# Optimization experiments

Measured on AMD Instinct MI355X. Metric: run time of the kernel, lower is better.

Reference implementation:

```python
import jax, jax.numpy as jnp
import numpy as np

S, NB, C = 7, 2, 20
LAMBDA_COORD, LAMBDA_NOOBJ = 5.0, 0.5
EPS = 1e-6


def _iou(a, b):
    """Midpoint-format IoU. a, b: [..., 4] = (x, y, w, h)."""
    ax1, ay1 = a[..., 0] - a[..., 2] / 2, a[..., 1] - a[..., 3] / 2
    ax2, ay2 = a[..., 0] + a[..., 2] / 2, a[..., 1] + a[..., 3] / 2
    bx1, by1 = b[..., 0] - b[..., 2] / 2, b[..., 1] - b[..., 3] / 2
    bx2, by2 = b[..., 0] + b[..., 2] / 2, b[..., 1] + b[..., 3] / 2
    iw = jnp.clip(jnp.minimum(ax2, bx2) - jnp.maximum(ax1, bx1), 0.0)
    ih = jnp.clip(jnp.minimum(ay2, by2) - jnp.maximum(ay1, by1), 0.0)
    inter = iw * ih
    area_a = jnp.abs((ax2 - ax1) * (ay2 - ay1))
    area_b = jnp.abs((bx2 - bx1) * (by2 - by1))
    return inter / (area_a + area_b - inter + EPS)


def setup_inputs() -> dict:
    key = jax.random.key(0)
    k1, k2, k3, k4 = jax.random.split(key, 4)
    N = 16384
    predictions = jax.random.uniform(k1, (N, S * S * (C + NB * 5)), dtype=jnp.float32)
    cls = jax.random.uniform(k2, (N, S, S, C), dtype=jnp.float32)
    box_rest = jax.random.uniform(k3, (N, S, S, 4), dtype=jnp.float32)  # y,w,h,conf
    u = jax.random.uniform(k4, (N, S, S, 2), dtype=jnp.float32)
    flag = jnp.where(u[..., 0] < 0.3, 1.0, u[..., 1] * 0.99)
    targets = jnp.concatenate([cls, flag[..., None], box_rest], axis=-1)  # [N,S,S,25]
    return {"predictions": predictions, "targets": targets}


def reference(predictions, targets):
    N = predictions.shape[0]
    pred = predictions.reshape(N, S, S, C + NB * 5)
    class_pred = pred[..., :C]                      # [N,S,S,20]
    b1 = pred[..., C:C + 5]                         # [N,S,S,5]
    b2 = pred[..., C + 5:C + 10]                    # [N,S,S,5]
    tbox = targets[..., C:C + 5]                    # [N,S,S,5]
    obj = (targets[..., C] == 1.0).astype(pred.dtype)  # [N,S,S]

    iou1 = _iou(b1[..., :4], tbox[..., :4])
    iou2 = _iou(b2[..., :4], tbox[..., :4])
    resp = jnp.where((iou1 > iou2)[..., None], b1, b2)  # responsible box [N,S,S,5]

    xy = (resp[..., 0] - tbox[..., 0]) ** 2 + (resp[..., 1] - tbox[..., 1]) ** 2
    wh = (jnp.sqrt(resp[..., 2]) - jnp.sqrt(tbox[..., 2])) ** 2 \
       + (jnp.sqrt(resp[..., 3]) - jnp.sqrt(tbox[..., 3])) ** 2
    coord = LAMBDA_COORD * (xy + wh)
    conf = (resp[..., 4] - tbox[..., 4]) ** 2
    cls_loss = jnp.sum((class_pred - targets[..., :C]) ** 2, axis=-1)

    obj_terms = jnp.sum(obj * (coord + conf + cls_loss))
    noobj_terms = LAMBDA_NOOBJ * jnp.sum((1.0 - obj) * (b1[..., 4] ** 2 + b2[..., 4] ** 2))
    return (obj_terms + noobj_terms) / N
```

## Files before the change

kernel.cpp:

```cpp
#include <hip/hip_runtime.h>
#include <math.h>

#define SS 7
#define CC 20
#define CELL_PRED 30
#define CELL_TGT  25
#define BLOCK 256

__device__ __forceinline__ float iou_box(const float* __restrict__ a,
                                         const float* __restrict__ b) {
    const float EPS = 1e-6f;
    float ax1 = a[0] - a[2] * 0.5f, ay1 = a[1] - a[3] * 0.5f;
    float ax2 = a[0] + a[2] * 0.5f, ay2 = a[1] + a[3] * 0.5f;
    float bx1 = b[0] - b[2] * 0.5f, by1 = b[1] - b[3] * 0.5f;
    float bx2 = b[0] + b[2] * 0.5f, by2 = b[1] + b[3] * 0.5f;
    float iw = fmaxf(fminf(ax2, bx2) - fmaxf(ax1, bx1), 0.0f);
    float ih = fmaxf(fminf(ay2, by2) - fmaxf(ay1, by1), 0.0f);
    float inter = iw * ih;
    float area_a = fabsf((ax2 - ax1) * (ay2 - ay1));
    float area_b = fabsf((bx2 - bx1) * (by2 - by1));
    return inter / (area_a + area_b - inter + EPS);
}

__global__ __launch_bounds__(BLOCK) void yolo_cell_loss(
    const float* __restrict__ pred,
    const float* __restrict__ tgt,
    float* __restrict__ partials,
    int nCells)
{
    __shared__ __align__(16) float s_pred[BLOCK * CELL_PRED];
    __shared__ __align__(16) float s_tgt [BLOCK * CELL_TGT];
    __shared__ float s_red[BLOCK / 64];

    const int tid = threadIdx.x;
    const int blockCell = blockIdx.x * BLOCK;
    const bool fullBlock = (blockCell + BLOCK) <= nCells;

    if (fullBlock) {
        const float4* gp = (const float4*)(pred + (size_t)blockCell * CELL_PRED);
        float4* sp = (float4*)s_pred;
        #pragma unroll
        for (int i = tid; i < BLOCK * CELL_PRED / 4; i += BLOCK) sp[i] = gp[i];
        const float4* gt = (const float4*)(tgt + (size_t)blockCell * CELL_TGT);
        float4* st = (float4*)s_tgt;
        #pragma unroll
        for (int i = tid; i < BLOCK * CELL_TGT / 4; i += BLOCK) st[i] = gt[i];
    } else {
        int nc = nCells - blockCell;
        if (nc < 0) nc = 0;
        for (int i = tid; i < nc * CELL_PRED; i += BLOCK)
            s_pred[i] = pred[(size_t)blockCell * CELL_PRED + i];
        for (int i = tid; i < nc * CELL_TGT; i += BLOCK)
            s_tgt[i] = tgt[(size_t)blockCell * CELL_TGT + i];
    }
    __syncthreads();

    float loss = 0.0f;
    const int cell = blockCell + tid;
    if (cell < nCells) {
        const float* p = s_pred + tid * CELL_PRED;
        const float* t = s_tgt  + tid * CELL_TGT;

        const float* b1 = p + CC;
        const float* b2 = p + CC + 5;
        const float* tb = t + CC;

        float obj = (tb[0] == 1.0f) ? 1.0f : 0.0f;

        float iou1 = iou_box(b1, tb);
        float iou2 = iou_box(b2, tb);
        bool pick1 = iou1 > iou2;
        float r0 = pick1 ? b1[0] : b2[0];
        float r1 = pick1 ? b1[1] : b2[1];
        float r2 = pick1 ? b1[2] : b2[2];
        float r3 = pick1 ? b1[3] : b2[3];
        float r4 = pick1 ? b1[4] : b2[4];

        float dx = r0 - tb[0], dy = r1 - tb[1];
        float xy = dx * dx + dy * dy;
        float dw = sqrtf(r2) - sqrtf(tb[2]);
        float dh = sqrtf(r3) - sqrtf(tb[3]);
        float wh = dw * dw + dh * dh;
        float coord = 5.0f * (xy + wh);
        float dconf = r4 - tb[4];
        float conf = dconf * dconf;

        float cls = 0.0f;
        #pragma unroll
        for (int k = 0; k < CC; ++k) {
            float d = p[k] - t[k];
            cls += d * d;
        }

        float noobj = 0.5f * (1.0f - obj) * (b1[4] * b1[4] + b2[4] * b2[4]);
        loss = obj * (coord + conf + cls) + noobj;
    }

    #pragma unroll
    for (int off = 32; off > 0; off >>= 1)
        loss += __shfl_down(loss, off, 64);
    if ((tid & 63) == 0) s_red[tid >> 6] = loss;
    __syncthreads();
    if (tid == 0) {
        float s = 0.0f;
        #pragma unroll
        for (int w = 0; w < BLOCK / 64; ++w) s += s_red[w];
        partials[blockIdx.x] = s;
    }
}

__global__ __launch_bounds__(BLOCK) void yolo_final_reduce(
    const float* __restrict__ partials, int nPartials, double invN,
    float* __restrict__ out)
{
    __shared__ double s_red[BLOCK / 64];
    double sum = 0.0;
    for (int i = threadIdx.x; i < nPartials; i += BLOCK)
        sum += (double)partials[i];
    #pragma unroll
    for (int off = 32; off > 0; off >>= 1)
        sum += __shfl_down(sum, off, 64);
    if ((threadIdx.x & 63) == 0) s_red[threadIdx.x >> 6] = sum;
    __syncthreads();
    if (threadIdx.x == 0) {
        double s = 0.0;
        #pragma unroll
        for (int w = 0; w < BLOCK / 64; ++w) s += s_red[w];
        out[0] = (float)(s * invN);
    }
}

extern "C" void kernel_launch(void* const* d_in, const int* in_sizes, int n_in,
                              void* d_out, int out_size, void* d_ws, size_t ws_size,
                              hipStream_t stream) {
    const float* pred = (const float*)d_in[0];
    const float* tgt  = (const float*)d_in[1];
    float* out = (float*)d_out;
    float* partials = (float*)d_ws;

    const int N = in_sizes[0] / (SS * SS * CELL_PRED);
    const int nCells = N * SS * SS;
    const int nBlocks = (nCells + BLOCK - 1) / BLOCK;

    yolo_cell_loss<<<nBlocks, BLOCK, 0, stream>>>(pred, tgt, partials, nCells);
    yolo_final_reduce<<<1, BLOCK, 0, stream>>>(partials, nBlocks, 1.0 / (double)N, out);
}
```

Before: 205.7 us.

## Use persistent grid with register-prefetched tiles and fused atomic final reduction

Replaces the one-block-per-256-cells launch with a fixed grid of 1280 blocks of 128 threads that loop over 128-cell tiles. Each block prefetches the next tile into registers while computing the current one from LDS, so global loads overlap compute. The separate final-reduce kernel is dropped in favour of a double atomicAdd plus a last-block counter, with a memset added to zero the workspace. It assumes nCells is a multiple of 128 and drops tail handling, and it adds an extra memset launch.

```diff
diff --git a/kernel.cpp b/kernel.cpp
--- a/kernel.cpp
+++ b/kernel.cpp
@@ -5,7 +5,13 @@
 #define CC 20
 #define CELL_PRED 30
 #define CELL_TGT  25
-#define BLOCK 256
+#define TILE 128
+#define BLOCK 128
+#define P4_PER_TILE (TILE * CELL_PRED / 4)
+#define T4_PER_TILE (TILE * CELL_TGT / 4)
+#define NPJ 8
+#define NTJ 7
+#define GRID 1280
 
 __device__ __forceinline__ float iou_box(const float* __restrict__ a,
                                          const float* __restrict__ b) {
@@ -22,111 +28,130 @@
     return inter / (area_a + area_b - inter + EPS);
 }
 
-__global__ __launch_bounds__(BLOCK) void yolo_cell_loss(
+__global__ __launch_bounds__(BLOCK) void yolo_loss_fused(
     const float* __restrict__ pred,
     const float* __restrict__ tgt,
-    float* __restrict__ partials,
-    int nCells)
+    float* __restrict__ out,
+    double* __restrict__ accum,
+    int* __restrict__ counter,
+    int nCells, int nTiles, double invN)
 {
-    __shared__ __align__(16) float s_pred[BLOCK * CELL_PRED];
-    __shared__ __align__(16) float s_tgt [BLOCK * CELL_TGT];
-    __shared__ float s_red[BLOCK / 64];
+    __shared__ __align__(16) float s_pred[TILE * CELL_PRED];
+    __shared__ __align__(16) float s_tgt [TILE * CELL_TGT];
+    __shared__ float s_red[2];
 
     const int tid = threadIdx.x;
-    const int blockCell = blockIdx.x * BLOCK;
-    const bool fullBlock = (blockCell + BLOCK) <= nCells;
 
-    if (fullBlock) {
-        const float4* gp = (const float4*)(pred + (size_t)blockCell * CELL_PRED);
-        float4* sp = (float4*)s_pred;
+    float4 rp[NPJ], rt[NTJ];
+
+    int t = blockIdx.x;
+    {
+        const float4* gp = (const float4*)pred + (size_t)t * P4_PER_TILE;
+        const float4* gt = (const float4*)tgt + (size_t)t * T4_PER_TILE;
         #pragma unroll
-        for (int i = tid; i < BLOCK * CELL_PRED / 4; i += BLOCK) sp[i] = gp[i];
-        const float4* gt = (const float4*)(tgt + (size_t)blockCell * CELL_TGT);
-        float4* st = (float4*)s_tgt;
+        for (int j = 0; j < NPJ; ++j) {
+            int idx = tid + j * BLOCK;
+            if (idx < P4_PER_TILE) rp[j] = gp[idx];
+        }
         #pragma unroll
-        for (int i = tid; i < BLOCK * CELL_TGT / 4; i += BLOCK) st[i] = gt[i];
-    } else {
-        int nc = nCells - blockCell;
-        if (nc < 0) nc = 0;
-        for (int i = tid; i < nc * CELL_PRED; i += BLOCK)
-            s_pred[i] = pred[(size_t)blockCell * CELL_PRED + i];
-        for (int i = tid; i < nc * CELL_TGT; i += BLOCK)
-            s_tgt[i] = tgt[(size_t)blockCell * CELL_TGT + i];
+        for (int j = 0; j < NTJ; ++j) {
+            int idx = tid + j * BLOCK;
+            if (idx < T4_PER_TILE) rt[j] = gt[idx];
+        }
     }
-    __syncthreads();
 
     float loss = 0.0f;
-    const int cell = blockCell + tid;
-    if (cell < nCells) {
-        const float* p = s_pred + tid * CELL_PRED;
-        const float* t = s_tgt  + tid * CELL_TGT;
 
-        const float* b1 = p + CC;
-        const float* b2 = p + CC + 5;
-        const float* tb = t + CC;
+    while (t < nTiles) {
+        __syncthreads();
+        {
+            float4* sp = (float4*)s_pred;
+            float4* st = (float4*)s_tgt;
+            #pragma unroll
+            for (int j = 0; j < NPJ; ++j) {
+                int idx = tid + j * BLOCK;
+                if (idx < P4_PER_TILE) sp[idx] = rp[j];
+            }
+            #pragma unroll
+            for (int j = 0; j < NTJ; ++j) {
+                int idx = tid + j * BLOCK;
+                if (idx < T4_PER_TILE) st[idx] = rt[j];
+            }
+        }
+        __syncthreads();
 
-        float obj = (tb[0] == 1.0f) ? 1.0f : 0.0f;
-
-        float iou1 = iou_box(b1, tb);
-        float iou2 = iou_box(b2, tb);
-        bool pick1 = iou1 > iou2;
-        float r0 = pick1 ? b1[0] : b2[0];
-        float r1 = pick1 ? b1[1] : b2[1];
-        float r2 = pick1 ? b1[2] : b2[2];
-        float r3 = pick1 ? b1[3] : b2[3];
-        float r4 = pick1 ? b1[4] : b2[4];
-
-        float dx = r0 - tb[0], dy = r1 - tb[1];
-        float xy = dx * dx + dy * dy;
-        float dw = sqrtf(r2) - sqrtf(tb[2]);
-        float dh = sqrtf(r3) - sqrtf(tb[3]);
-        float wh = dw * dw + dh * dh;
-        float coord = 5.0f * (xy + wh);
-        float dconf = r4 - tb[4];
-        float conf = dconf * dconf;
-
-        float cls = 0.0f;
-        #pragma unroll
-        for (int k = 0; k < CC; ++k) {
-            float d = p[k] - t[k];
-            cls += d * d;
+        int tn = t + GRID;
+        if (tn < nTiles) {
+            const float4* gp = (const float4*)pred + (size_t)tn * P4_PER_TILE;
+            const float4* gt = (const float4*)tgt + (size_t)tn * T4_PER_TILE;
+            #pragma unroll
+            for (int j = 0; j < NPJ; ++j) {
+                int idx = tid + j * BLOCK;
+                if (idx < P4_PER_TILE) rp[j] = gp[idx];
+            }
+            #pragma unroll
+            for (int j = 0; j < NTJ; ++j) {
+                int idx = tid + j * BLOCK;
+                if (idx < T4_PER_TILE) rt[j] = gt[idx];
+            }
         }
 
-        float noobj = 0.5f * (1.0f - obj) * (b1[4] * b1[4] + b2[4] * b2[4]);
-        loss = obj * (coord + conf + cls) + noobj;
+        {
+            const float* p = s_pred + tid * CELL_PRED;
+            const float* tt = s_tgt + tid * CELL_TGT;
+            const float* b1 = p + CC;
+            const float* b2 = p + CC + 5;
+            const float* tb = tt + CC;
+
+            float obj = (tb[0] == 1.0f) ? 1.0f : 0.0f;
+
+            float iou1 = iou_box(b1, tb);
+            float iou2 = iou_box(b2, tb);
+            bool pick1 = iou1 > iou2;
+            float r0 = pick1 ? b1[0] : b2[0];
+            float r1 = pick1 ? b1[1] : b2[1];
+            float r2 = pick1 ? b1[2] : b2[2];
+            float r3 = pick1 ? b1[3] : b2[3];
+            float r4 = pick1 ? b1[4] : b2[4];
+
+            float dx = r0 - tb[0], dy = r1 - tb[1];
+            float xy = dx * dx + dy * dy;
+            float dw = sqrtf(r2) - sqrtf(tb[2]);
+            float dh = sqrtf(r3) - sqrtf(tb[3]);
+            float wh = dw * dw + dh * dh;
+            float coord = 5.0f * (xy + wh);
+            float dconf = r4 - tb[4];
+            float conf = dconf * dconf;
+
+            float cls = 0.0f;
+            #pragma unroll
+            for (int k = 0; k < CC; ++k) {
+                float d = p[k] - tt[k];
+                cls += d * d;
+            }
+
+            float noobj = 0.5f * (1.0f - obj) * (b1[4] * b1[4] + b2[4] * b2[4]);
+            loss += obj * (coord + conf + cls) + noobj;
+        }
+        t = tn;
     }
 
     #pragma unroll
     for (int off = 32; off > 0; off >>= 1)
         loss += __shfl_down(loss, off, 64);
+    __syncthreads();
     if ((tid & 63) == 0) s_red[tid >> 6] = loss;
     __syncthreads();
+
     if (tid == 0) {
-        float s = 0.0f;
-        #pragma unroll
-        for (int w = 0; w < BLOCK / 64; ++w) s += s_red[w];
-        partials[blockIdx.x] = s;
-    }
-}
-
-__global__ __launch_bounds__(BLOCK) void yolo_final_reduce(
-    const float* __restrict__ partials, int nPartials, double invN,
-    float* __restrict__ out)
-{
-    __shared__ double s_red[BLOCK / 64];
-    double sum = 0.0;
-    for (int i = threadIdx.x; i < nPartials; i += BLOCK)
-        sum += (double)partials[i];
-    #pragma unroll
-    for (int off = 32; off > 0; off >>= 1)
-        sum += __shfl_down(sum, off, 64);
-    if ((threadIdx.x & 63) == 0) s_red[threadIdx.x >> 6] = sum;
-    __syncthreads();
-    if (threadIdx.x == 0) {
-        double s = 0.0;
-        #pragma unroll
-        for (int w = 0; w < BLOCK / 64; ++w) s += s_red[w];
-        out[0] = (float)(s * invN);
+        double part = (double)s_red[0] + (double)s_red[1];
+        atomicAdd(accum, part);
+        __threadfence();
+        int old = atomicAdd(counter, 1);
+        if (old == GRID - 1) {
+            double total = atomicAdd(accum, 0.0);
+            out[0] = (float)(total * invN);
+        }
     }
 }
 
@@ -136,12 +161,14 @@
     const float* pred = (const float*)d_in[0];
     const float* tgt  = (const float*)d_in[1];
     float* out = (float*)d_out;
-    float* partials = (float*)d_ws;
+    double* accum = (double*)d_ws;
+    int* counter = (int*)((char*)d_ws + 8);
 
     const int N = in_sizes[0] / (SS * SS * CELL_PRED);
     const int nCells = N * SS * SS;
-    const int nBlocks = (nCells + BLOCK - 1) / BLOCK;
+    const int nTiles = nCells / TILE;
 
-    yolo_cell_loss<<<nBlocks, BLOCK, 0, stream>>>(pred, tgt, partials, nCells);
-    yolo_final_reduce<<<1, BLOCK, 0, stream>>>(partials, nBlocks, 1.0 / (double)N, out);
+    hipMemsetAsync(d_ws, 0, 16, stream);
+    yolo_loss_fused<<<GRID, BLOCK, 0, stream>>>(
+        pred, tgt, out, accum, counter, nCells, nTiles, 1.0 / (double)N);
 }
```

After: 304.3 us. 1.48x slower.
